# Kernel optimization log

Measured on AMD Instinct MI355X. Metric: run time of the kernel, lower is better.

Reference implementation:

```python
import jax, jax.numpy as jnp
import numpy as np

N_BINS = 64
N_SPLINE_DIMS = 3 * N_BINS - 1
N_GENES = 5000
N_GENES_OI = 5000
N_CUTS = 500_000
WINDOW_A, WINDOW_B = -10000.0, 10000.0
AB = WINDOW_B - WINDOW_A
MIN_BIN_WIDTH = 1e-3
MIN_BIN_HEIGHT = 1e-3
MIN_DERIVATIVE = 1e-3
# default init so that softplus(init) + min_derivative == 1 at the tails
DEFAULT_INIT = float(np.log(np.exp(1.0 - MIN_DERIVATIVE) - 1.0))
LOG_HALF = float(np.log(0.5))
LOG_AB = float(np.log(AB))


def setup_inputs() -> dict:
    key = jax.random.key(0)
    k1, k2, k3, k4 = jax.random.split(key, 4)
    value = jax.random.uniform(k1, (N_CUTS,), minval=WINDOW_A, maxval=WINDOW_B, dtype=jnp.float32)
    delta_spline = jax.random.normal(k2, (N_CUTS, N_SPLINE_DIMS), dtype=jnp.float32) * 0.1
    genes_oi = jax.random.randint(k3, (N_GENES_OI,), 0, N_GENES, dtype=jnp.int64 if jax.config.jax_enable_x64 else jnp.int32)
    local_gene_ix = jax.random.randint(k4, (N_CUTS,), 0, N_GENES_OI, dtype=jnp.int64 if jax.config.jax_enable_x64 else jnp.int32)
    spline_weight = jnp.full((N_GENES, N_SPLINE_DIMS), DEFAULT_INIT, dtype=jnp.float32)
    return {"value": value, "delta_spline": delta_spline, "genes_oi": genes_oi,
            "local_gene_ix": local_gene_ix, "spline_weight": spline_weight}


def _rqs_inverse(x, uw, uh, ud_padded):
    """Rational-quadratic spline, inverse pass, domain [-1,1]x[-1,1].
    x: (N,1); uw, uh: (N,1,K); ud_padded: (N,1,K+1)."""
    K = uw.shape[-1]
    pad = [(0, 0)] * (uw.ndim - 1) + [(1, 0)]

    w = jax.nn.softmax(uw, axis=-1)
    w = MIN_BIN_WIDTH + (1.0 - MIN_BIN_WIDTH * K) * w
    cw = jnp.pad(jnp.cumsum(w, axis=-1), pad)
    cw = 2.0 * cw - 1.0  # map [0,1] -> [-1,1]
    cw = cw.at[..., 0].set(-1.0).at[..., -1].set(1.0)
    w = cw[..., 1:] - cw[..., :-1]

    d = MIN_DERIVATIVE + jax.nn.softplus(ud_padded)  # (N,1,K+1)

    h = jax.nn.softmax(uh, axis=-1)
    h = MIN_BIN_HEIGHT + (1.0 - MIN_BIN_HEIGHT * K) * h
    ch = jnp.pad(jnp.cumsum(h, axis=-1), pad)
    ch = 2.0 * ch - 1.0
    ch = ch.at[..., 0].set(-1.0).at[..., -1].set(1.0)
    h = ch[..., 1:] - ch[..., :-1]

    # searchsorted over cumulative heights (inverse pass)
    bins = ch.at[..., -1].add(1e-6)
    idx = jnp.clip(jnp.sum((x[..., None] >= bins).astype(jnp.int32), axis=-1) - 1, 0, K - 1)

    def gather(t):
        return jnp.take_along_axis(t, idx[..., None], axis=-1)[..., 0]

    in_cw = gather(cw)
    in_w = gather(w)
    in_ch = gather(ch)
    in_h = gather(h)
    delta = gather(h / w)
    d0 = gather(d)
    d1 = jnp.take_along_axis(d, (idx + 1)[..., None], axis=-1)[..., 0]

    dy = x - in_ch
    s = d0 + d1 - 2.0 * delta
    a = dy * s + in_h * (delta - d0)
    b = in_h * d0 - dy * s
    c = -delta * dy
    disc = b * b - 4.0 * a * c
    root = (2.0 * c) / (-b - jnp.sqrt(jnp.maximum(disc, 0.0)))  # theta in [0,1]
    y = root * in_w + in_cw

    tom = root * (1.0 - root)
    denom = delta + s * tom
    deriv_num = (delta * delta) * (d1 * root * root + 2.0 * delta * tom + d0 * (1.0 - root) * (1.0 - root))
    logabsdet = -(jnp.log(deriv_num) - 2.0 * jnp.log(denom))  # negated for inverse
    return y, logabsdet


def reference(value, delta_spline, genes_oi, local_gene_ix, spline_weight):
    K = N_BINS
    spline = spline_weight[genes_oi][local_gene_ix] + delta_spline  # (N, 3K-1)
    uw = spline[:, None, :K]           # (N,1,K)
    uh = spline[:, None, K:2 * K]      # (N,1,K)
    ud = spline[:, None, 2 * K:]       # (N,1,K-1)

    x = (((value - WINDOW_A) / AB) - 0.5) * 2.0  # normalize to [-1,1]
    x = x[:, None]  # (N,1)

    inside = (x >= -1.0) & (x <= 1.0)
    ud_padded = jnp.pad(ud, [(0, 0), (0, 0), (1, 1)], constant_values=DEFAULT_INIT)
    xc = jnp.clip(x, -1.0, 1.0)
    _, logdet = _rqs_inverse(xc, uw, uh, ud_padded)
    logdet = jnp.where(inside, logdet, 0.0)  # linear tails: logabsdet = 0
    return LOG_HALF + logdet - LOG_AB  # (N,1)
```

## Files before the change

### kernel.cpp

```cpp
#include <hip/hip_runtime.h>

#define K_BINS 64
#define N_SPLINE 191
constexpr float MIN_BIN_WIDTH  = 0.001f;
constexpr float MIN_BIN_HEIGHT = 0.001f;
constexpr float MIN_DERIV      = 0.001f;
constexpr float WINDOW_A = -10000.0f;
constexpr float AB       = 20000.0f;
constexpr float LOG_HALF = -0.69314718055994530942f;
constexpr float LOG_AB   = 9.90348755253612804622f;

__global__ __launch_bounds__(256) void rqs_logdet_kernel(
    const float* __restrict__ value,
    const float* __restrict__ delta_spline,
    const int*   __restrict__ genes_oi,
    const int*   __restrict__ local_gene_ix,
    const float* __restrict__ spline_weight,
    float*       __restrict__ out,
    int n_cuts)
{
    const int lane = threadIdx.x & 63;
    const int wave = threadIdx.x >> 6;
    const int i = blockIdx.x * (blockDim.x >> 6) + wave;
    if (i >= n_cuts) return;

    const int g = genes_oi[local_gene_ix[i]];
    const float* __restrict__ sw = spline_weight + (long)g * N_SPLINE;
    const float* __restrict__ ds = delta_spline  + (long)i * N_SPLINE;

    const float uw  = sw[lane]       + ds[lane];
    const float uh  = sw[64 + lane]  + ds[64 + lane];
    const float udv = sw[127 + lane] + ds[127 + lane];

    const float ew = __expf(uw);
    const float eh = __expf(uh);
    float sum_w = ew, sum_h = eh;
    #pragma unroll
    for (int m = 1; m < 64; m <<= 1) {
        sum_w += __shfl_xor(sum_w, m, 64);
        sum_h += __shfl_xor(sum_h, m, 64);
    }
    const float wk = fmaf(ew, __fdividef(1.0f - MIN_BIN_WIDTH  * K_BINS, sum_w), MIN_BIN_WIDTH);
    const float hk = fmaf(eh, __fdividef(1.0f - MIN_BIN_HEIGHT * K_BINS, sum_h), MIN_BIN_HEIGHT);

    float pw = wk, ph = hk;
    #pragma unroll
    for (int off = 1; off < 64; off <<= 1) {
        const float tw = __shfl_up(pw, off, 64);
        const float th = __shfl_up(ph, off, 64);
        if (lane >= off) { pw += tw; ph += th; }
    }

    const float cw_r = (lane == 63) ?  1.0f : fmaf(2.0f, pw, -1.0f);
    const float cw_l = fmaf(2.0f, pw - wk, -1.0f);
    const float ch_r = (lane == 63) ?  1.0f : fmaf(2.0f, ph, -1.0f);
    const float ch_l = fmaf(2.0f, ph - hk, -1.0f);
    const float wbin = cw_r - cw_l;
    const float hbin = ch_r - ch_l;

    const float v = value[i];
    float x = fmaf(v - WINDOW_A, 2.0f / AB, -1.0f);
    const bool inside = (x >= -1.0f) && (x <= 1.0f);
    x = fminf(fmaxf(x, -1.0f), 1.0f);

    const unsigned long long ball = __ballot(x >= ch_r) & 0x7FFFFFFFFFFFFFFFull;
    const int idx = __popcll(ball);

    const float dval = (lane == 0) ? 1.0f
                     : (MIN_DERIV + __logf(1.0f + __expf(udv)));

    const float in_cw = __shfl(cw_l, idx, 64);  (void)in_cw;
    const float in_w  = __shfl(wbin, idx, 64);  (void)in_w;
    const float in_ch = __shfl(ch_l, idx, 64);
    const float in_h  = __shfl(hbin, idx, 64);
    const float d0    = __shfl(dval, idx, 64);
    const float d1    = (idx == 63) ? 1.0f : __shfl(dval, idx + 1, 64);

    const float delta = __fdividef(in_h, in_w);
    const float dy = x - in_ch;
    const float s2 = d0 + d1 - 2.0f * delta;
    const float aa = dy * s2 + in_h * (delta - d0);
    const float bb = in_h * d0 - dy * s2;
    const float cc = -delta * dy;
    const float disc = bb * bb - 4.0f * aa * cc;
    const float root = __fdividef(2.0f * cc, -bb - sqrtf(fmaxf(disc, 0.0f)));
    const float tom = root * (1.0f - root);
    const float denom = delta + s2 * tom;
    const float omr = 1.0f - root;
    const float dnum = delta * delta * (d1 * root * root + 2.0f * delta * tom + d0 * omr * omr);
    const float logabsdet = -(__logf(dnum) - 2.0f * __logf(denom));

    if (lane == 0)
        out[i] = LOG_HALF + (inside ? logabsdet : 0.0f) - LOG_AB;
}

extern "C" void kernel_launch(void* const* d_in, const int* in_sizes, int n_in,
                              void* d_out, int out_size, void* d_ws, size_t ws_size,
                              hipStream_t stream) {
    const float* value         = (const float*)d_in[0];
    const float* delta_spline  = (const float*)d_in[1];
    const int*   genes_oi      = (const int*)d_in[2];
    const int*   local_gene_ix = (const int*)d_in[3];
    const float* spline_weight = (const float*)d_in[4];
    float* out = (float*)d_out;

    const int n_cuts = in_sizes[0];
    const int waves_per_block = 4;
    const int blocks = (n_cuts + waves_per_block - 1) / waves_per_block;
    rqs_logdet_kernel<<<blocks, 256, 0, stream>>>(
        value, delta_spline, genes_oi, local_gene_ix, spline_weight, out, n_cuts);
}
```

Measured before the change: 589.6 us.

## Replace wave shuffles with DPP inclusive scan and scalar readlane gathers

The butterfly sum and shfl_up prefix scan are replaced by one DPP-based inclusive scan of the raw exponentials per row. The total comes from lane 63, and the cumulative widths and heights are rebuilt algebraically from the scaled scan plus the min-width term. Because the bin index is wave-uniform, the gathers of bin parameters use readlane instead of LDS-backed shuffles. The value load is also hoisted earlier. This aims to cut cross-lane latency and LDS traffic, at the cost of relying on DPP row-broadcast semantics and slightly different float rounding in the cumulative sums.

After: 552.9 us. 6.2% less time.

```diff
diff --git a/kernel.cpp b/kernel.cpp
--- a/kernel.cpp
+++ b/kernel.cpp
@@ -9,6 +9,26 @@
 constexpr float AB       = 20000.0f;
 constexpr float LOG_HALF = -0.69314718055994530942f;
 constexpr float LOG_AB   = 9.90348755253612804622f;
+
+template<int CTRL, int ROW_MASK>
+__device__ __forceinline__ float dpp_add(float x) {
+    int t = __builtin_amdgcn_update_dpp(0, __float_as_int(x), CTRL, ROW_MASK, 0xf, true);
+    return x + __int_as_float(t);
+}
+
+__device__ __forceinline__ float wave64_inclusive_scan(float x) {
+    x = dpp_add<0x111, 0xf>(x);
+    x = dpp_add<0x112, 0xf>(x);
+    x = dpp_add<0x114, 0xf>(x);
+    x = dpp_add<0x118, 0xf>(x);
+    x = dpp_add<0x142, 0xa>(x);
+    x = dpp_add<0x143, 0xc>(x);
+    return x;
+}
+
+__device__ __forceinline__ float readlane_f(float x, int lane) {
+    return __int_as_float(__builtin_amdgcn_readlane(__float_as_int(x), lane));
+}
 
 __global__ __launch_bounds__(256) void rqs_logdet_kernel(
     const float* __restrict__ value,
@@ -25,6 +45,8 @@
     if (i >= n_cuts) return;
 
     const int g = genes_oi[local_gene_ix[i]];
+    const float v = value[i];
+
     const float* __restrict__ sw = spline_weight + (long)g * N_SPLINE;
     const float* __restrict__ ds = delta_spline  + (long)i * N_SPLINE;
 
@@ -34,47 +56,42 @@
 
     const float ew = __expf(uw);
     const float eh = __expf(uh);
-    float sum_w = ew, sum_h = eh;
-    #pragma unroll
-    for (int m = 1; m < 64; m <<= 1) {
-        sum_w += __shfl_xor(sum_w, m, 64);
-        sum_h += __shfl_xor(sum_h, m, 64);
-    }
-    const float wk = fmaf(ew, __fdividef(1.0f - MIN_BIN_WIDTH  * K_BINS, sum_w), MIN_BIN_WIDTH);
-    const float hk = fmaf(eh, __fdividef(1.0f - MIN_BIN_HEIGHT * K_BINS, sum_h), MIN_BIN_HEIGHT);
 
-    float pw = wk, ph = hk;
-    #pragma unroll
-    for (int off = 1; off < 64; off <<= 1) {
-        const float tw = __shfl_up(pw, off, 64);
-        const float th = __shfl_up(ph, off, 64);
-        if (lane >= off) { pw += tw; ph += th; }
-    }
+    const float Ew = wave64_inclusive_scan(ew);
+    const float Eh = wave64_inclusive_scan(eh);
+    const float Sw = readlane_f(Ew, 63);
+    const float Sh = readlane_f(Eh, 63);
 
-    const float cw_r = (lane == 63) ?  1.0f : fmaf(2.0f, pw, -1.0f);
+    const float wsc = __fdividef(1.0f - MIN_BIN_WIDTH  * K_BINS, Sw);
+    const float hsc = __fdividef(1.0f - MIN_BIN_HEIGHT * K_BINS, Sh);
+
+    const float wk = fmaf(ew, wsc, MIN_BIN_WIDTH);
+    const float hk = fmaf(eh, hsc, MIN_BIN_HEIGHT);
+    const float pw = fmaf(Ew, wsc, MIN_BIN_WIDTH  * (float)(lane + 1));
+    const float ph = fmaf(Eh, hsc, MIN_BIN_HEIGHT * (float)(lane + 1));
+
+    const float cw_r = (lane == 63) ? 1.0f : fmaf(2.0f, pw, -1.0f);
     const float cw_l = fmaf(2.0f, pw - wk, -1.0f);
-    const float ch_r = (lane == 63) ?  1.0f : fmaf(2.0f, ph, -1.0f);
+    const float ch_r = (lane == 63) ? 1.0f : fmaf(2.0f, ph, -1.0f);
     const float ch_l = fmaf(2.0f, ph - hk, -1.0f);
     const float wbin = cw_r - cw_l;
     const float hbin = ch_r - ch_l;
 
-    const float v = value[i];
     float x = fmaf(v - WINDOW_A, 2.0f / AB, -1.0f);
     const bool inside = (x >= -1.0f) && (x <= 1.0f);
     x = fminf(fmaxf(x, -1.0f), 1.0f);
 
     const unsigned long long ball = __ballot(x >= ch_r) & 0x7FFFFFFFFFFFFFFFull;
-    const int idx = __popcll(ball);
+    const int idx = (int)__popcll(ball);
 
     const float dval = (lane == 0) ? 1.0f
                      : (MIN_DERIV + __logf(1.0f + __expf(udv)));
 
-    const float in_cw = __shfl(cw_l, idx, 64);  (void)in_cw;
-    const float in_w  = __shfl(wbin, idx, 64);  (void)in_w;
-    const float in_ch = __shfl(ch_l, idx, 64);
-    const float in_h  = __shfl(hbin, idx, 64);
-    const float d0    = __shfl(dval, idx, 64);
-    const float d1    = (idx == 63) ? 1.0f : __shfl(dval, idx + 1, 64);
+    const float in_w  = readlane_f(wbin, idx);
+    const float in_ch = readlane_f(ch_l, idx);
+    const float in_h  = readlane_f(hbin, idx);
+    const float d0    = readlane_f(dval, idx);
+    const float d1    = readlane_f(dval, (idx + 1) & 63);
 
     const float delta = __fdividef(in_h, in_w);
     const float dy = x - in_ch;
```

## Switch to one-thread-per-cut with LDS-transposed spline tile loads

Applied to the files above, without the earlier changes.

Replaces the one-wave-per-cut design with one thread per cut. The first 128 spline columns are staged through a padded shared-memory tile so global reads stay coalesced, and each thread does its own softmax sums and a serial 63-step search over cumulative heights. Only the selected bin's width and the two neighbouring derivative entries are recomputed, so softplus is no longer evaluated for all 64 bins. This removes the wave shuffles and ballots, but adds heavy register pressure (a 64-entry array), a large LDS tile that limits occupancy, and serial per-thread loops.

After: 585.7 us. No clear change (-0.7%).

```diff
diff --git a/kernel.cpp b/kernel.cpp
--- a/kernel.cpp
+++ b/kernel.cpp
@@ -1,96 +1,128 @@
 #include <hip/hip_runtime.h>
 
-#define K_BINS 64
-#define N_SPLINE 191
-constexpr float MIN_BIN_WIDTH  = 0.001f;
-constexpr float MIN_BIN_HEIGHT = 0.001f;
-constexpr float MIN_DERIV      = 0.001f;
-constexpr float WINDOW_A = -10000.0f;
-constexpr float AB       = 20000.0f;
+#define NSPL 191
+constexpr float MIN_W = 0.001f, MIN_H = 0.001f, MIN_D = 0.001f;
+constexpr float W_A = -10000.0f, AB = 20000.0f;
 constexpr float LOG_HALF = -0.69314718055994530942f;
 constexpr float LOG_AB   = 9.90348755253612804622f;
 
-__global__ __launch_bounds__(256) void rqs_logdet_kernel(
+#define CPB 256
+#define TC  32
+#define PITCH 33
+
+__global__ __launch_bounds__(CPB, 3) void rqs_tpc_kernel(
     const float* __restrict__ value,
-    const float* __restrict__ delta_spline,
+    const float* __restrict__ dsg,
     const int*   __restrict__ genes_oi,
-    const int*   __restrict__ local_gene_ix,
-    const float* __restrict__ spline_weight,
-    float*       __restrict__ out,
-    int n_cuts)
+    const int*   __restrict__ lgi,
+    const float* __restrict__ sw,
+    float* __restrict__ out, int n)
 {
-    const int lane = threadIdx.x & 63;
-    const int wave = threadIdx.x >> 6;
-    const int i = blockIdx.x * (blockDim.x >> 6) + wave;
-    if (i >= n_cuts) return;
+    __shared__ float tile[CPB * PITCH];
 
-    const int g = genes_oi[local_gene_ix[i]];
-    const float* __restrict__ sw = spline_weight + (long)g * N_SPLINE;
-    const float* __restrict__ ds = delta_spline  + (long)i * N_SPLINE;
+    const int t  = threadIdx.x;
+    const int i0 = blockIdx.x * CPB;
+    const int i  = i0 + t;
+    const int ic = min(i, n - 1);
 
-    const float uw  = sw[lane]       + ds[lane];
-    const float uh  = sw[64 + lane]  + ds[64 + lane];
-    const float udv = sw[127 + lane] + ds[127 + lane];
+    const int g = genes_oi[lgi[ic]];
+    const float* __restrict__ swr = sw  + (long)g  * NSPL;
+    const float* __restrict__ dsr = dsg + (long)ic * NSPL;
 
-    const float ew = __expf(uw);
-    const float eh = __expf(uh);
-    float sum_w = ew, sum_h = eh;
-    #pragma unroll
-    for (int m = 1; m < 64; m <<= 1) {
-        sum_w += __shfl_xor(sum_w, m, 64);
-        sum_h += __shfl_xor(sum_h, m, 64);
-    }
-    const float wk = fmaf(ew, __fdividef(1.0f - MIN_BIN_WIDTH  * K_BINS, sum_w), MIN_BIN_WIDTH);
-    const float hk = fmaf(eh, __fdividef(1.0f - MIN_BIN_HEIGHT * K_BINS, sum_h), MIN_BIN_HEIGHT);
-
-    float pw = wk, ph = hk;
-    #pragma unroll
-    for (int off = 1; off < 64; off <<= 1) {
-        const float tw = __shfl_up(pw, off, 64);
-        const float th = __shfl_up(ph, off, 64);
-        if (lane >= off) { pw += tw; ph += th; }
-    }
-
-    const float cw_r = (lane == 63) ?  1.0f : fmaf(2.0f, pw, -1.0f);
-    const float cw_l = fmaf(2.0f, pw - wk, -1.0f);
-    const float ch_r = (lane == 63) ?  1.0f : fmaf(2.0f, ph, -1.0f);
-    const float ch_l = fmaf(2.0f, ph - hk, -1.0f);
-    const float wbin = cw_r - cw_l;
-    const float hbin = ch_r - ch_l;
-
-    const float v = value[i];
-    float x = fmaf(v - WINDOW_A, 2.0f / AB, -1.0f);
+    const float v = value[ic];
+    float x = fmaf(v - W_A, 2.0f / AB, -1.0f);
     const bool inside = (x >= -1.0f) && (x <= 1.0f);
     x = fminf(fmaxf(x, -1.0f), 1.0f);
 
-    const unsigned long long ball = __ballot(x >= ch_r) & 0x7FFFFFFFFFFFFFFFull;
-    const int idx = __popcll(ball);
+    float eh[64];
+    float s0 = 0.f, s1 = 0.f, s2a = 0.f, s3 = 0.f;
+    float h0 = 0.f, h1 = 0.f, h2a = 0.f, h3 = 0.f;
 
-    const float dval = (lane == 0) ? 1.0f
-                     : (MIN_DERIV + __logf(1.0f + __expf(udv)));
+    const int c  = t & (TC - 1);
+    const int r0 = t >> 5;
 
-    const float in_cw = __shfl(cw_l, idx, 64);  (void)in_cw;
-    const float in_w  = __shfl(wbin, idx, 64);  (void)in_w;
-    const float in_ch = __shfl(ch_l, idx, 64);
-    const float in_h  = __shfl(hbin, idx, 64);
-    const float d0    = __shfl(dval, idx, 64);
-    const float d1    = (idx == 63) ? 1.0f : __shfl(dval, idx + 1, 64);
+    #pragma unroll
+    for (int tt = 0; tt < 4; ++tt) {
+        const int jc = tt * TC;
+
+        float tmp[32];
+        #pragma unroll
+        for (int rr = 0; rr < 32; ++rr) {
+            const int r  = r0 + (rr << 3);
+            const int rg = min(i0 + r, n - 1);
+            tmp[rr] = dsg[(long)rg * NSPL + jc + c];
+        }
+        #pragma unroll
+        for (int rr = 0; rr < 32; ++rr) {
+            const int r = r0 + (rr << 3);
+            tile[r * PITCH + c] = tmp[rr];
+        }
+        __syncthreads();
+
+        #pragma unroll
+        for (int j = 0; j < TC; ++j) {
+            const float u = tile[t * PITCH + j] + swr[jc + j];
+            const float e = __expf(u);
+            if (tt < 2) {
+                if ((j & 3) == 0) s0 += e;
+                else if ((j & 3) == 1) s1 += e;
+                else if ((j & 3) == 2) s2a += e;
+                else s3 += e;
+            } else {
+                eh[jc + j - 64] = e;
+                if ((j & 3) == 0) h0 += e;
+                else if ((j & 3) == 1) h1 += e;
+                else if ((j & 3) == 2) h2a += e;
+                else h3 += e;
+            }
+        }
+        __syncthreads();
+    }
+
+    const float Sw = (s0 + s1) + (s2a + s3);
+    const float Sh = (h0 + h1) + (h2a + h3);
+    const float wsc2 = 2.0f * __fdividef(1.0f - MIN_W * 64.0f, Sw);
+    const float hsc2 = 2.0f * __fdividef(1.0f - MIN_H * 64.0f, Sh);
+
+    float Eh = 0.0f, capEh = 0.0f;
+    int idx = 0;
+    #pragma unroll
+    for (int j = 0; j < 63; ++j) {
+        Eh += eh[j];
+        const float chr = fmaf(hsc2, Eh, 2.0f * MIN_H * (float)(j + 1) - 1.0f);
+        const bool take = (x >= chr);
+        idx  += take ? 1 : 0;
+        capEh = take ? Eh : capEh;
+    }
+
+    const float ew_i = __expf(dsr[idx]      + swr[idx]);
+    const float eh_i = __expf(dsr[64 + idx] + swr[64 + idx]);
+    const int c0 = 127 + max(idx, 1);
+    const int c1 = 128 + min(idx, 62);
+    const float u0 = dsr[c0] + swr[c0];
+    const float u1 = dsr[c1] + swr[c1];
+    const float d0 = (idx == 0)  ? 1.0f : (MIN_D + __logf(1.0f + __expf(u0)));
+    const float d1 = (idx == 63) ? 1.0f : (MIN_D + __logf(1.0f + __expf(u1)));
+
+    const float in_w = fmaf(wsc2, ew_i, 2.0f * MIN_W);
+    const float in_h = fmaf(hsc2, eh_i, 2.0f * MIN_H);
+    const float ch_l = fmaf(hsc2, capEh, fmaf(2.0f * MIN_H, (float)idx, -1.0f));
 
     const float delta = __fdividef(in_h, in_w);
-    const float dy = x - in_ch;
-    const float s2 = d0 + d1 - 2.0f * delta;
-    const float aa = dy * s2 + in_h * (delta - d0);
-    const float bb = in_h * d0 - dy * s2;
+    const float dy = x - ch_l;
+    const float ss = d0 + d1 - 2.0f * delta;
+    const float aa = dy * ss + in_h * (delta - d0);
+    const float bb = in_h * d0 - dy * ss;
     const float cc = -delta * dy;
     const float disc = bb * bb - 4.0f * aa * cc;
     const float root = __fdividef(2.0f * cc, -bb - sqrtf(fmaxf(disc, 0.0f)));
     const float tom = root * (1.0f - root);
-    const float denom = delta + s2 * tom;
+    const float denom = delta + ss * tom;
     const float omr = 1.0f - root;
     const float dnum = delta * delta * (d1 * root * root + 2.0f * delta * tom + d0 * omr * omr);
     const float logabsdet = -(__logf(dnum) - 2.0f * __logf(denom));
 
-    if (lane == 0)
+    if (i < n)
         out[i] = LOG_HALF + (inside ? logabsdet : 0.0f) - LOG_AB;
 }
 
@@ -104,9 +136,8 @@
     const float* spline_weight = (const float*)d_in[4];
     float* out = (float*)d_out;
 
-    const int n_cuts = in_sizes[0];
-    const int waves_per_block = 4;
-    const int blocks = (n_cuts + waves_per_block - 1) / waves_per_block;
-    rqs_logdet_kernel<<<blocks, 256, 0, stream>>>(
-        value, delta_spline, genes_oi, local_gene_ix, spline_weight, out, n_cuts);
+    const int n = in_sizes[0];
+    const int blocks = (n + CPB - 1) / CPB;
+    rqs_tpc_kernel<<<blocks, CPB, 0, stream>>>(
+        value, delta_spline, genes_oi, local_gene_ix, spline_weight, out, n);
 }
```
